# Performance work log

Measured on AMD Instinct MI355X. Metric: run time of the kernel, lower is better.

Reference implementation:

```python
import jax, jax.numpy as jnp
import numpy as np

B, N, C_IN = 8, 2048, 3
D = 64            # graph-conv feature dim
SPARSE_K = 8      # k_neighbors(16) * sparse_ratio(0.5)
LEVELS = 3        # wavelet_levels
H1, H2 = 256, 128 # fusion hidden dims

def _lin(key, fan_in, fan_out):
    k1, k2 = jax.random.split(key)
    s = 1.0 / np.sqrt(fan_in)
    W = jax.random.uniform(k1, (fan_in, fan_out), minval=-s, maxval=s, dtype=jnp.float32)
    b = jax.random.uniform(k2, (fan_out,), minval=-s, maxval=s, dtype=jnp.float32)
    return W, b

def setup_inputs() -> dict:
    key = jax.random.key(0)
    ks = jax.random.split(key, 12)
    x = jax.random.normal(ks[0], (B, N, C_IN), dtype=jnp.float32)
    W1, b1 = _lin(ks[1], C_IN, D)          # feature_transform
    W2, b2 = _lin(ks[2], 2 * D, D)         # edge_conv
    Ws1, bs1 = _lin(ks[3], C_IN, 64)       # suppressor layer 1
    Ws2, bs2 = _lin(ks[4], 64, LEVELS)     # suppressor layer 2
    Wf1, bf1 = _lin(ks[5], D * LEVELS, H1) # fusion
    Wf2, bf2 = _lin(ks[6], H1, H2)
    Wf3, bf3 = _lin(ks[7], H2, C_IN)
    ones = jnp.ones; zeros = jnp.zeros
    return {
        'x': x,
        'W1': W1, 'b1': b1, 'g1': ones((D,), jnp.float32), 'be1': zeros((D,), jnp.float32),
        'W2': W2, 'b2': b2, 'g2': ones((D,), jnp.float32), 'be2': zeros((D,), jnp.float32),
        'Ws1': Ws1, 'bs1': bs1, 'Ws2': Ws2, 'bs2': bs2,
        'Wf1': Wf1, 'bf1': bf1, 'gf1': ones((H1,), jnp.float32), 'bef1': zeros((H1,), jnp.float32),
        'Wf2': Wf2, 'bf2': bf2, 'gf2': ones((H2,), jnp.float32), 'bef2': zeros((H2,), jnp.float32),
        'Wf3': Wf3, 'bf3': bf3,
    }

def _leaky(v):
    return jnp.where(v > 0, v, 0.2 * v)

def reference(x, W1, b1, g1, be1, W2, b2, g2, be2, Ws1, bs1, Ws2, bs2,
              Wf1, bf1, gf1, bef1, Wf2, bf2, gf2, bef2, Wf3, bf3):
    # ---- AdaptiveSparseGraphConv ----
    # feature transform + eval-mode BN (running mean 0 / var 1 -> affine)
    feat = _leaky((x @ W1 + b1) * g1 + be1)                     # [B,N,D]
    # KNN via squared distances (monotonic in true cdist)
    x2 = jnp.sum(x * x, axis=-1)                                # [B,N]
    d2 = x2[:, :, None] + x2[:, None, :] - 2.0 * jnp.einsum('bnc,bmc->bnm', x, x)
    _, idx = jax.lax.top_k(-d2, SPARSE_K)                       # [B,N,k] nearest
    neighbor = jax.vmap(lambda f, i: f[i])(feat, idx)           # [B,N,k,D]
    edge = jnp.concatenate(
        [jnp.broadcast_to(feat[:, :, None, :], neighbor.shape), neighbor], axis=-1)  # [B,N,k,2D]
    conv = _leaky((edge @ W2 + b2) * g2 + be2)                  # [B,N,k,D]
    agg = jnp.max(conv, axis=2)                                 # [B,N,D]
    # ---- AdaptiveFrequencySupressor (per-point wavelet-level weights) ----
    fw = jax.nn.sigmoid(jax.nn.relu(x @ Ws1 + bs1) @ Ws2 + bs2) # [B,N,LEVELS]
    # frequency-adaptive multi-level weighting, concat across levels
    multi = (agg[:, :, None, :] * fw[:, :, :, None]).reshape(B, N, LEVELS * D)  # [B,N,LEVELS*D]
    # ---- EnhancedMultiScaleFusion (eval: dropout off, BN affine) ----
    h = _leaky((multi @ Wf1 + bf1) * gf1 + bef1)
    h = _leaky((h @ Wf2 + bf2) * gf2 + bef2)
    delta = h @ Wf3 + bf3                                       # [B,N,3]
    # ---- residual regularized output ----
    return x + 0.1 * delta
```

## Files before the change

kernel.cpp:

```cpp
#include <hip/hip_runtime.h>
#include <hip/hip_bf16.h>
#include <math.h>

#define BB   8
#define NN   2048
#define BN   16384
#define KNB  8

__device__ __forceinline__ float leaky(float v){ return v > 0.f ? v : 0.2f*v; }

using bf16x8 = __attribute__((ext_vector_type(8))) short;
using f32x16 = __attribute__((ext_vector_type(16))) float;

__global__ __launch_bounds__(256) void k_prep(
    const float* __restrict__ x,
    const float* __restrict__ Ws1, const float* __restrict__ bs1,
    const float* __restrict__ Ws2, const float* __restrict__ bs2,
    const float* __restrict__ Wf1, const float* __restrict__ Wf2,
    float* __restrict__ fw, __hip_bfloat16* __restrict__ Wf1T,
    __hip_bfloat16* __restrict__ Wf2T)
{
    int t = threadIdx.x;
    if (blockIdx.x < 4096) {
        int lane = t & 63;
        int p = blockIdx.x * 4 + (t >> 6);
        float x0 = x[p*3+0], x1 = x[p*3+1], x2 = x[p*3+2];
        int d = lane;
        float h = x0*Ws1[d] + x1*Ws1[64+d] + x2*Ws1[128+d] + bs1[d];
        h = fmaxf(h, 0.f);
        float s[3];
        #pragma unroll
        for (int l = 0; l < 3; ++l) {
            float v = h * Ws2[d*3 + l];
            #pragma unroll
            for (int off = 32; off; off >>= 1) v += __shfl_xor(v, off, 64);
            s[l] = v;
        }
        if (lane < 3) fw[p*3 + lane] = 1.f / (1.f + expf(-(s[lane] + bs2[lane])));
    } else if (blockIdx.x < 4120) {
        int base = (blockIdx.x - 4096) * 2048 + t * 8;
        #pragma unroll
        for (int j = 0; j < 8; ++j) {
            int e = base + j;
            int n = e / 192, k = e % 192;
            Wf1T[e] = __float2bfloat16(Wf1[k*256 + n]);
        }
    } else {
        int base = (blockIdx.x - 4120) * 2048 + t * 8;
        #pragma unroll
        for (int j = 0; j < 8; ++j) {
            int e = base + j;
            int n = e / 256, k = e % 256;
            Wf2T[e] = __float2bfloat16(Wf2[k*128 + n]);
        }
    }
}

#define CE64(a, b) { bool c_ = (b) < (a); unsigned long long mn_ = c_ ? (b) : (a); \
                     unsigned long long mx_ = c_ ? (a) : (b); (a) = mn_; (b) = mx_; }

__global__ __launch_bounds__(1024, 8) void k_knn(const float* __restrict__ x, int* __restrict__ idxo)
{
    __shared__ __align__(16) char smem[65536];
    float4*   sp  = (float4*)smem;
    unsigned* khi = (unsigned*)smem;
    unsigned* klo = (unsigned*)(smem + 32768);

    int t = threadIdx.x;
    int b = blockIdx.x >> 6;
    int qbase = (blockIdx.x & 63) * 32;
    int q = t & 31, seg = t >> 5;

    for (int i = t; i < NN; i += 1024) {
        float a = x[(b*NN + i)*3 + 0];
        float c = x[(b*NN + i)*3 + 1];
        float e = x[(b*NN + i)*3 + 2];
        sp[i] = make_float4(a, c, e, a*a + c*c + e*e);
    }
    __syncthreads();

    float4 qv = sp[qbase + q];

    unsigned long long R[8];
    #pragma unroll
    for (int j = 0; j < 8; ++j) R[j] = 0xFFFFFFFFFFFFFFFFull;

    int m0 = seg * 64;
    #pragma unroll 2
    for (int g = 0; g < 8; ++g) {
        unsigned long long S[8];
        #pragma unroll
        for (int jj = 0; jj < 8; ++jj) {
            int m = m0 + g*8 + jj;
            float4 v = sp[m];
            float s = qv.x*v.x; s = fmaf(qv.y, v.y, s); s = fmaf(qv.z, v.z, s);
            float d2 = fmaf(-2.f, s, qv.w + v.w);
            unsigned ub = __float_as_uint(d2);
            unsigned u  = ub ^ (unsigned)(((int)ub >> 31) | 0x80000000);
            S[jj] = ((unsigned long long)u << 32) | (unsigned)m;
        }
        CE64(S[0],S[1]); CE64(S[2],S[3]); CE64(S[4],S[5]); CE64(S[6],S[7]);
        CE64(S[0],S[2]); CE64(S[1],S[3]); CE64(S[4],S[6]); CE64(S[5],S[7]);
        CE64(S[1],S[2]); CE64(S[5],S[6]);
        CE64(S[0],S[4]); CE64(S[1],S[5]); CE64(S[2],S[6]); CE64(S[3],S[7]);
        CE64(S[2],S[4]); CE64(S[3],S[5]);
        CE64(S[1],S[2]); CE64(S[3],S[4]); CE64(S[5],S[6]);
        #pragma unroll
        for (int j = 0; j < 8; ++j) {
            unsigned long long bb = S[7-j];
            R[j] = R[j] < bb ? R[j] : bb;
        }
        CE64(R[0],R[4]); CE64(R[1],R[5]); CE64(R[2],R[6]); CE64(R[3],R[7]);
        CE64(R[0],R[2]); CE64(R[1],R[3]); CE64(R[4],R[6]); CE64(R[5],R[7]);
        CE64(R[0],R[1]); CE64(R[2],R[3]); CE64(R[4],R[5]); CE64(R[6],R[7]);
    }

    __syncthreads();
    #pragma unroll
    for (int j = 0; j < 8; ++j) {
        khi[j*1024 + t] = (unsigned)(R[j] >> 32);
        klo[j*1024 + t] = (unsigned)R[j];
    }

    for (int L = 32; L >= 2; L >>= 1) {
        __syncthreads();
        unsigned long long A[8], Bv[8];
        int p = t >> 5;
        bool active = (p < (L >> 1));
        if (active) {
            int rowA = (2*p)*32 + q, rowB = (2*p + 1)*32 + q;
            #pragma unroll
            for (int j = 0; j < 8; ++j) {
                A[j]  = ((unsigned long long)khi[j*1024 + rowA] << 32) | klo[j*1024 + rowA];
                Bv[j] = ((unsigned long long)khi[j*1024 + rowB] << 32) | klo[j*1024 + rowB];
            }
        }
        __syncthreads();
        if (active) {
            unsigned long long C[8];
            #pragma unroll
            for (int j = 0; j < 8; ++j) {
                unsigned long long bb = Bv[7-j];
                C[j] = A[j] < bb ? A[j] : bb;
            }
            CE64(C[0],C[4]); CE64(C[1],C[5]); CE64(C[2],C[6]); CE64(C[3],C[7]);
            CE64(C[0],C[2]); CE64(C[1],C[3]); CE64(C[4],C[6]); CE64(C[5],C[7]);
            CE64(C[0],C[1]); CE64(C[2],C[3]); CE64(C[4],C[5]); CE64(C[6],C[7]);
            if (L > 2) {
                int rowO = p*32 + q;
                #pragma unroll
                for (int j = 0; j < 8; ++j) {
                    khi[j*1024 + rowO] = (unsigned)(C[j] >> 32);
                    klo[j*1024 + rowO] = (unsigned)C[j];
                }
            } else {
                #pragma unroll
                for (int j = 0; j < 8; ++j)
                    idxo[(b*NN + qbase + q)*KNB + j] = b*NN + (int)(C[j] & 0xFFFFFFFFu);
            }
        }
    }
}

__global__ __launch_bounds__(256) void k_pq(
    const float* __restrict__ x,
    const float* __restrict__ W1, const float* __restrict__ b1,
    const float* __restrict__ g1, const float* __restrict__ be1,
    const float* __restrict__ W2, float* __restrict__ PQ)
{
    __shared__ float F_s[64*66];
    __shared__ float W_s[32*132];

    int t = threadIdx.x;
    int rb = blockIdx.x * 64;

    {
        int d = t & 63, g = t >> 6;
        float w0 = W1[d], w1 = W1[64+d], w2 = W1[128+d];
        float bb = b1[d], gg = g1[d], ee = be1[d];
        #pragma unroll 4
        for (int i = 0; i < 16; ++i) {
            int r = g*16 + i;
            const float* xp = &x[(rb + r)*3];
            float f = xp[0]*w0 + xp[1]*w1 + xp[2]*w2 + bb;
            f = leaky(f*gg + ee);
            F_s[r*66 + d] = f;
        }
    }

    int tx = t & 15, ty = t >> 4;
    float acc[4][8];
    #pragma unroll
    for (int i = 0; i < 4; ++i)
        #pragma unroll
        for (int j = 0; j < 8; ++j) acc[i][j] = 0.f;

    for (int k0 = 0; k0 < 64; k0 += 32) {
        __syncthreads();
        #pragma unroll
        for (int it = 0; it < 2; ++it) {
            int i2 = t + it*256;
            int k = i2 >> 4, c8 = (i2 & 15) * 8;
            const float* src = &W2[(k0 + k + (c8 >= 64 ? 64 : 0))*64 + (c8 & 63)];
            *(float4*)&W_s[k*132 + c8]     = *(const float4*)src;
            *(float4*)&W_s[k*132 + c8 + 4] = *(const float4*)(src + 4);
        }
        __syncthreads();
        #pragma unroll 4
        for (int kk = 0; kk < 32; ++kk) {
            float a[4];
            #pragma unroll
            for (int i = 0; i < 4; ++i) a[i] = F_s[(ty*4 + i)*66 + k0 + kk];
            float4 wA = *(const float4*)&W_s[kk*132 + tx*8];
            float4 wB = *(const float4*)&W_s[kk*132 + tx*8 + 4];
            #pragma unroll
            for (int i = 0; i < 4; ++i) {
                acc[i][0] = fmaf(a[i], wA.x, acc[i][0]);
                acc[i][1] = fmaf(a[i], wA.y, acc[i][1]);
                acc[i][2] = fmaf(a[i], wA.z, acc[i][2]);
                acc[i][3] = fmaf(a[i], wA.w, acc[i][3]);
                acc[i][4] = fmaf(a[i], wB.x, acc[i][4]);
                acc[i][5] = fmaf(a[i], wB.y, acc[i][5]);
                acc[i][6] = fmaf(a[i], wB.z, acc[i][6]);
                acc[i][7] = fmaf(a[i], wB.w, acc[i][7]);
            }
        }
    }

    #pragma unroll
    for (int i = 0; i < 4; ++i) {
        int r = rb + ty*4 + i;
        *(float4*)&PQ[r*128 + tx*8]     = make_float4(acc[i][0], acc[i][1], acc[i][2], acc[i][3]);
        *(float4*)&PQ[r*128 + tx*8 + 4] = make_float4(acc[i][4], acc[i][5], acc[i][6], acc[i][7]);
    }
}

__global__ __launch_bounds__(256) void k_agg(
    const float* __restrict__ PQ, const int* __restrict__ idx,
    const float* __restrict__ fw,
    const float* __restrict__ b2, const float* __restrict__ g2, const float* __restrict__ be2,
    __hip_bfloat16* __restrict__ multi)
{
    int lane = threadIdx.x & 63;
    int p = blockIdx.x * 4 + (threadIdx.x >> 6);
    float Pv = PQ[p*128 + lane] + b2[lane];
    float g = g2[lane], be = be2[lane];
    float mx = -1e30f;
    #pragma unroll
    for (int j = 0; j < KNB; ++j) {
        int nb = idx[p*KNB + j];
        float v = (Pv + PQ[nb*128 + 64 + lane]) * g + be;
        mx = fmaxf(mx, leaky(v));
    }
    float w0 = fw[p*3+0], w1 = fw[p*3+1], w2 = fw[p*3+2];
    multi[p*192 + lane]       = __float2bfloat16(mx * w0);
    multi[p*192 + 64  + lane] = __float2bfloat16(mx * w1);
    multi[p*192 + 128 + lane] = __float2bfloat16(mx * w2);
}

__global__ __launch_bounds__(256) void k_h1(
    const ushort* __restrict__ multi, const ushort* __restrict__ Wf1T,
    const float* __restrict__ bf1, const float* __restrict__ gf1,
    const float* __restrict__ bef1, __hip_bfloat16* __restrict__ h1)
{
    __shared__ ushort A_s[128*72];
    __shared__ ushort B_s[64*72];

    int t = threadIdx.x, w = t >> 6, lane = t & 63;
    int rb = blockIdx.x * 128, cb = blockIdx.y * 64;

    f32x16 acc[2];
    #pragma unroll
    for (int i = 0; i < 16; ++i) { acc[0][i] = 0.f; acc[1][i] = 0.f; }

    for (int k0 = 0; k0 < 192; k0 += 64) {
        #pragma unroll
        for (int it = 0; it < 4; ++it) {
            int i = t + it*256; int r = i >> 3, kq = (i & 7)*8;
            *(uint4*)&A_s[r*72 + kq] = *(const uint4*)&multi[(rb + r)*192 + k0 + kq];
        }
        #pragma unroll
        for (int it = 0; it < 2; ++it) {
            int i = t + it*256; int n = i >> 3, kq = (i & 7)*8;
            *(uint4*)&B_s[n*72 + kq] = *(const uint4*)&Wf1T[(cb + n)*192 + k0 + kq];
        }
        __syncthreads();
        int row = w*32 + (lane & 31);
        int kb = (lane >> 5)*8;
        #pragma unroll
        for (int s = 0; s < 4; ++s) {
            bf16x8 a  = *(const bf16x8*)&A_s[row*72 + s*16 + kb];
            bf16x8 b0 = *(const bf16x8*)&B_s[(lane & 31)*72 + s*16 + kb];
            bf16x8 b1 = *(const bf16x8*)&B_s[(32 + (lane & 31))*72 + s*16 + kb];
            acc[0] = __builtin_amdgcn_mfma_f32_32x32x16_bf16(a, b0, acc[0], 0, 0, 0);
            acc[1] = __builtin_amdgcn_mfma_f32_32x32x16_bf16(a, b1, acc[1], 0, 0, 0);
        }
        __syncthreads();
    }

    #pragma unroll
    for (int nb = 0; nb < 2; ++nb) {
        int c = cb + nb*32 + (lane & 31);
        float bv = bf1[c], gv = gf1[c], ev = bef1[c];
        #pragma unroll
        for (int r16 = 0; r16 < 16; ++r16) {
            int rr = (r16 & 3) + 8*(r16 >> 2) + 4*(lane >> 5);
            float v = leaky((acc[nb][r16] + bv)*gv + ev);
            h1[(rb + w*32 + rr)*256 + c] = __float2bfloat16(v);
        }
    }
}

__global__ __launch_bounds__(256) void k_h2out(
    const ushort* __restrict__ h1, const ushort* __restrict__ Wf2T,
    const float* __restrict__ bf2, const float* __restrict__ gf2,
    const float* __restrict__ bef2,
    const float* __restrict__ Wf3, const float* __restrict__ bf3,
    const float* __restrict__ x, float* __restrict__ out)
{
    __shared__ ushort A_s[128*72];
    __shared__ ushort B_s[128*72];

    int t = threadIdx.x, w = t >> 6, lane = t & 63;
    int rb = blockIdx.x * 128;

    f32x16 acc[4];
    #pragma unroll
    for (int nb = 0; nb < 4; ++nb)
        #pragma unroll
        for (int i = 0; i < 16; ++i) acc[nb][i] = 0.f;

    for (int k0 = 0; k0 < 256; k0 += 64) {
        #pragma unroll
        for (int it = 0; it < 4; ++it) {
            int i = t + it*256; int r = i >> 3, kq = (i & 7)*8;
            *(uint4*)&A_s[r*72 + kq] = *(const uint4*)&h1[(rb + r)*256 + k0 + kq];
        }
        #pragma unroll
        for (int it = 0; it < 4; ++it) {
            int i = t + it*256; int n = i >> 3, kq = (i & 7)*8;
            *(uint4*)&B_s[n*72 + kq] = *(const uint4*)&Wf2T[n*256 + k0 + kq];
        }
        __syncthreads();
        int row = w*32 + (lane & 31);
        int kb = (lane >> 5)*8;
        #pragma unroll
        for (int s = 0; s < 4; ++s) {
            bf16x8 a = *(const bf16x8*)&A_s[row*72 + s*16 + kb];
            #pragma unroll
            for (int nb = 0; nb < 4; ++nb) {
                bf16x8 b = *(const bf16x8*)&B_s[(nb*32 + (lane & 31))*72 + s*16 + kb];
                acc[nb] = __builtin_amdgcn_mfma_f32_32x32x16_bf16(a, b, acc[nb], 0, 0, 0);
            }
        }
        __syncthreads();
    }

    float bv[4], gv[4], ev[4], w3[4][3];
    #pragma unroll
    for (int nb = 0; nb < 4; ++nb) {
        int c = nb*32 + (lane & 31);
        bv[nb] = bf2[c]; gv[nb] = gf2[c]; ev[nb] = bef2[c];
        #pragma unroll
        for (int l = 0; l < 3; ++l) w3[nb][l] = Wf3[c*3 + l];
    }
    float b30 = bf3[0], b31 = bf3[1], b32 = bf3[2];

    #pragma unroll
    for (int r16 = 0; r16 < 16; ++r16) {
        float d0 = 0.f, d1 = 0.f, d2 = 0.f;
        #pragma unroll
        for (int nb = 0; nb < 4; ++nb) {
            float v = leaky((acc[nb][r16] + bv[nb])*gv[nb] + ev[nb]);
            d0 = fmaf(v, w3[nb][0], d0);
            d1 = fmaf(v, w3[nb][1], d1);
            d2 = fmaf(v, w3[nb][2], d2);
        }
        #pragma unroll
        for (int off = 16; off; off >>= 1) {
            d0 += __shfl_xor(d0, off, 64);
            d1 += __shfl_xor(d1, off, 64);
            d2 += __shfl_xor(d2, off, 64);
        }
        int row = rb + w*32 + (r16 & 3) + 8*(r16 >> 2) + 4*(lane >> 5);
        int l = lane & 31;
        if (l < 3) {
            float dl = (l == 0) ? d0 : (l == 1 ? d1 : d2);
            float bl = (l == 0) ? b30 : (l == 1 ? b31 : b32);
            out[row*3 + l] = x[row*3 + l] + 0.1f*(dl + bl);
        }
    }
}

extern "C" void kernel_launch(void* const* d_in, const int* in_sizes, int n_in,
                              void* d_out, int out_size, void* d_ws, size_t ws_size,
                              hipStream_t stream)
{
    const float* x    = (const float*)d_in[0];
    const float* W1   = (const float*)d_in[1];
    const float* b1   = (const float*)d_in[2];
    const float* g1   = (const float*)d_in[3];
    const float* be1  = (const float*)d_in[4];
    const float* W2   = (const float*)d_in[5];
    const float* b2   = (const float*)d_in[6];
    const float* g2   = (const float*)d_in[7];
    const float* be2  = (const float*)d_in[8];
    const float* Ws1  = (const float*)d_in[9];
    const float* bs1  = (const float*)d_in[10];
    const float* Ws2  = (const float*)d_in[11];
    const float* bs2  = (const float*)d_in[12];
    const float* Wf1  = (const float*)d_in[13];
    const float* bf1  = (const float*)d_in[14];
    const float* gf1  = (const float*)d_in[15];
    const float* bef1 = (const float*)d_in[16];
    const float* Wf2  = (const float*)d_in[17];
    const float* bf2  = (const float*)d_in[18];
    const float* gf2  = (const float*)d_in[19];
    const float* bef2 = (const float*)d_in[20];
    const float* Wf3  = (const float*)d_in[21];
    const float* bf3  = (const float*)d_in[22];
    float* out = (float*)d_out;

    char* ws = (char*)d_ws;
    float*          fw    = (float*)         (ws + 0);
    int*            idx   = (int*)           (ws + (1u  << 20));
    __hip_bfloat16* Wf1T  = (__hip_bfloat16*)(ws + (2u  << 20));
    __hip_bfloat16* Wf2T  = (__hip_bfloat16*)(ws + (3u  << 20));
    float*          PQ    = (float*)         (ws + (4u  << 20));
    __hip_bfloat16* multi = (__hip_bfloat16*)(ws + (12u << 20));
    __hip_bfloat16* h1    = (__hip_bfloat16*)(ws + (20u << 20));

    k_prep<<<4136, 256, 0, stream>>>(x, Ws1, bs1, Ws2, bs2, Wf1, Wf2, fw, Wf1T, Wf2T);
    k_knn<<<BB*64, 1024, 0, stream>>>(x, idx);
    k_pq<<<BN/64, 256, 0, stream>>>(x, W1, b1, g1, be1, W2, PQ);
    k_agg<<<BN/4, 256, 0, stream>>>(PQ, idx, fw, b2, g2, be2, multi);
    k_h1<<<dim3(BN/128, 4), 256, 0, stream>>>((const ushort*)multi, (const ushort*)Wf1T,
                                              bf1, gf1, bef1, h1);
    k_h2out<<<dim3(BN/128, 1), 256, 0, stream>>>((const ushort*)h1, (const ushort*)Wf2T,
                                                 bf2, gf2, bef2, Wf3, bf3, x, out);
}
```

Before: 180.5 us.

## Fuse prep into pq and agg kernels, store gathered Q half in bf16

Removes the standalone prep kernel: weight transposes move into extra blocks of the pq kernel, and the suppressor MLP that computes per-point level weights is computed inline in the aggregation kernel. The Q half of the edge-conv projection, which is gathered per neighbour, is stored in bf16 to halve gather traffic, while P stays fp32. The KNN key encoding is simplified by clamping distances to non-negative so the raw float bits sort correctly. This cuts one launch and the fw and PQ memory traffic, at the cost of bf16 rounding on neighbour features and recomputing the MLP per point in the aggregation kernel.

```diff
diff --git a/kernel.cpp b/kernel.cpp
--- a/kernel.cpp
+++ b/kernel.cpp
@@ -9,49 +9,118 @@
 
 __device__ __forceinline__ float leaky(float v){ return v > 0.f ? v : 0.2f*v; }
 
+__device__ __forceinline__ ushort f2bf(float f){
+    unsigned u = __float_as_uint(f);
+    return (ushort)((u + 0x7FFFu + ((u >> 16) & 1u)) >> 16);
+}
+__device__ __forceinline__ float bf2f(ushort h){
+    return __uint_as_float(((unsigned)h) << 16);
+}
+
 using bf16x8 = __attribute__((ext_vector_type(8))) short;
 using f32x16 = __attribute__((ext_vector_type(16))) float;
 
-__global__ __launch_bounds__(256) void k_prep(
+__global__ __launch_bounds__(256) void k_pq(
     const float* __restrict__ x,
-    const float* __restrict__ Ws1, const float* __restrict__ bs1,
-    const float* __restrict__ Ws2, const float* __restrict__ bs2,
+    const float* __restrict__ W1, const float* __restrict__ b1,
+    const float* __restrict__ g1, const float* __restrict__ be1,
+    const float* __restrict__ W2,
     const float* __restrict__ Wf1, const float* __restrict__ Wf2,
-    float* __restrict__ fw, __hip_bfloat16* __restrict__ Wf1T,
-    __hip_bfloat16* __restrict__ Wf2T)
+    float* __restrict__ P, ushort* __restrict__ Qb,
+    ushort* __restrict__ Wf1T, ushort* __restrict__ Wf2T)
 {
     int t = threadIdx.x;
-    if (blockIdx.x < 4096) {
-        int lane = t & 63;
-        int p = blockIdx.x * 4 + (t >> 6);
-        float x0 = x[p*3+0], x1 = x[p*3+1], x2 = x[p*3+2];
-        int d = lane;
-        float h = x0*Ws1[d] + x1*Ws1[64+d] + x2*Ws1[128+d] + bs1[d];
-        h = fmaxf(h, 0.f);
-        float s[3];
-        #pragma unroll
-        for (int l = 0; l < 3; ++l) {
-            float v = h * Ws2[d*3 + l];
-            #pragma unroll
-            for (int off = 32; off; off >>= 1) v += __shfl_xor(v, off, 64);
-            s[l] = v;
-        }
-        if (lane < 3) fw[p*3 + lane] = 1.f / (1.f + expf(-(s[lane] + bs2[lane])));
-    } else if (blockIdx.x < 4120) {
-        int base = (blockIdx.x - 4096) * 2048 + t * 8;
-        #pragma unroll
-        for (int j = 0; j < 8; ++j) {
-            int e = base + j;
-            int n = e / 192, k = e % 192;
-            Wf1T[e] = __float2bfloat16(Wf1[k*256 + n]);
-        }
-    } else {
-        int base = (blockIdx.x - 4120) * 2048 + t * 8;
-        #pragma unroll
-        for (int j = 0; j < 8; ++j) {
-            int e = base + j;
-            int n = e / 256, k = e % 256;
-            Wf2T[e] = __float2bfloat16(Wf2[k*128 + n]);
+    int bid = blockIdx.x;
+    if (bid >= 256) {
+        if (bid < 280) {
+            int base = (bid - 256) * 2048 + t * 8;
+            #pragma unroll
+            for (int j = 0; j < 8; ++j) {
+                int e = base + j;
+                int n = e / 192, k = e % 192;
+                Wf1T[e] = f2bf(Wf1[k*256 + n]);
+            }
+        } else {
+            int base = (bid - 280) * 2048 + t * 8;
+            #pragma unroll
+            for (int j = 0; j < 8; ++j) {
+                int e = base + j;
+                int n = e / 256, k = e % 256;
+                Wf2T[e] = f2bf(Wf2[k*128 + n]);
+            }
+        }
+        return;
+    }
+
+    __shared__ float F_s[64*66];
+    __shared__ float W_s[32*132];
+
+    int rb = bid * 64;
+
+    {
+        int d = t & 63, g = t >> 6;
+        float w0 = W1[d], w1 = W1[64+d], w2 = W1[128+d];
+        float bb = b1[d], gg = g1[d], ee = be1[d];
+        #pragma unroll 4
+        for (int i = 0; i < 16; ++i) {
+            int r = g*16 + i;
+            const float* xp = &x[(rb + r)*3];
+            float f = xp[0]*w0 + xp[1]*w1 + xp[2]*w2 + bb;
+            f = leaky(f*gg + ee);
+            F_s[r*66 + d] = f;
+        }
+    }
+
+    int tx = t & 15, ty = t >> 4;
+    float acc[4][8];
+    #pragma unroll
+    for (int i = 0; i < 4; ++i)
+        #pragma unroll
+        for (int j = 0; j < 8; ++j) acc[i][j] = 0.f;
+
+    for (int k0 = 0; k0 < 64; k0 += 32) {
+        __syncthreads();
+        #pragma unroll
+        for (int it = 0; it < 2; ++it) {
+            int i2 = t + it*256;
+            int k = i2 >> 4, c8 = (i2 & 15) * 8;
+            const float* src = &W2[(k0 + k + (c8 >= 64 ? 64 : 0))*64 + (c8 & 63)];
+            *(float4*)&W_s[k*132 + c8]     = *(const float4*)src;
+            *(float4*)&W_s[k*132 + c8 + 4] = *(const float4*)(src + 4);
+        }
+        __syncthreads();
+        #pragma unroll 4
+        for (int kk = 0; kk < 32; ++kk) {
+            float a[4];
+            #pragma unroll
+            for (int i = 0; i < 4; ++i) a[i] = F_s[(ty*4 + i)*66 + k0 + kk];
+            float4 wA = *(const float4*)&W_s[kk*132 + tx*8];
+            float4 wB = *(const float4*)&W_s[kk*132 + tx*8 + 4];
+            #pragma unroll
+            for (int i = 0; i < 4; ++i) {
+                acc[i][0] = fmaf(a[i], wA.x, acc[i][0]);
+                acc[i][1] = fmaf(a[i], wA.y, acc[i][1]);
+                acc[i][2] = fmaf(a[i], wA.z, acc[i][2]);
+                acc[i][3] = fmaf(a[i], wA.w, acc[i][3]);
+                acc[i][4] = fmaf(a[i], wB.x, acc[i][4]);
+                acc[i][5] = fmaf(a[i], wB.y, acc[i][5]);
+                acc[i][6] = fmaf(a[i], wB.z, acc[i][6]);
+                acc[i][7] = fmaf(a[i], wB.w, acc[i][7]);
+            }
+        }
+    }
+
+    #pragma unroll
+    for (int i = 0; i < 4; ++i) {
+        int r = rb + ty*4 + i;
+        if (tx < 8) {
+            *(float4*)&P[r*64 + tx*8]     = make_float4(acc[i][0], acc[i][1], acc[i][2], acc[i][3]);
+            *(float4*)&P[r*64 + tx*8 + 4] = make_float4(acc[i][4], acc[i][5], acc[i][6], acc[i][7]);
+        } else {
+            union { ushort u[8]; uint4 v; } pk;
+            #pragma unroll
+            for (int j = 0; j < 8; ++j) pk.u[j] = f2bf(acc[i][j]);
+            *(uint4*)&Qb[r*64 + (tx - 8)*8] = pk.v;
         }
     }
 }
@@ -95,8 +164,7 @@
             float4 v = sp[m];
             float s = qv.x*v.x; s = fmaf(qv.y, v.y, s); s = fmaf(qv.z, v.z, s);
             float d2 = fmaf(-2.f, s, qv.w + v.w);
-            unsigned ub = __float_as_uint(d2);
-            unsigned u  = ub ^ (unsigned)(((int)ub >> 31) | 0x80000000);
+            unsigned u = __float_as_uint(fmaxf(d2, 0.f));
             S[jj] = ((unsigned long long)u << 32) | (unsigned)m;
         }
         CE64(S[0],S[1]); CE64(S[2],S[3]); CE64(S[4],S[5]); CE64(S[6],S[7]);
@@ -162,106 +230,52 @@
     }
 }
 
-__global__ __launch_bounds__(256) void k_pq(
+__global__ __launch_bounds__(256) void k_agg(
     const float* __restrict__ x,
-    const float* __restrict__ W1, const float* __restrict__ b1,
-    const float* __restrict__ g1, const float* __restrict__ be1,
-    const float* __restrict__ W2, float* __restrict__ PQ)
-{
-    __shared__ float F_s[64*66];
-    __shared__ float W_s[32*132];
-
-    int t = threadIdx.x;
-    int rb = blockIdx.x * 64;
-
-    {
-        int d = t & 63, g = t >> 6;
-        float w0 = W1[d], w1 = W1[64+d], w2 = W1[128+d];
-        float bb = b1[d], gg = g1[d], ee = be1[d];
-        #pragma unroll 4
-        for (int i = 0; i < 16; ++i) {
-            int r = g*16 + i;
-            const float* xp = &x[(rb + r)*3];
-            float f = xp[0]*w0 + xp[1]*w1 + xp[2]*w2 + bb;
-            f = leaky(f*gg + ee);
-            F_s[r*66 + d] = f;
-        }
-    }
-
-    int tx = t & 15, ty = t >> 4;
-    float acc[4][8];
-    #pragma unroll
-    for (int i = 0; i < 4; ++i)
-        #pragma unroll
-        for (int j = 0; j < 8; ++j) acc[i][j] = 0.f;
-
-    for (int k0 = 0; k0 < 64; k0 += 32) {
-        __syncthreads();
-        #pragma unroll
-        for (int it = 0; it < 2; ++it) {
-            int i2 = t + it*256;
-            int k = i2 >> 4, c8 = (i2 & 15) * 8;
-            const float* src = &W2[(k0 + k + (c8 >= 64 ? 64 : 0))*64 + (c8 & 63)];
-            *(float4*)&W_s[k*132 + c8]     = *(const float4*)src;
-            *(float4*)&W_s[k*132 + c8 + 4] = *(const float4*)(src + 4);
-        }
-        __syncthreads();
-        #pragma unroll 4
-        for (int kk = 0; kk < 32; ++kk) {
-            float a[4];
-            #pragma unroll
-            for (int i = 0; i < 4; ++i) a[i] = F_s[(ty*4 + i)*66 + k0 + kk];
-            float4 wA = *(const float4*)&W_s[kk*132 + tx*8];
-            float4 wB = *(const float4*)&W_s[kk*132 + tx*8 + 4];
-            #pragma unroll
-            for (int i = 0; i < 4; ++i) {
-                acc[i][0] = fmaf(a[i], wA.x, acc[i][0]);
-                acc[i][1] = fmaf(a[i], wA.y, acc[i][1]);
-                acc[i][2] = fmaf(a[i], wA.z, acc[i][2]);
-                acc[i][3] = fmaf(a[i], wA.w, acc[i][3]);
-                acc[i][4] = fmaf(a[i], wB.x, acc[i][4]);
-                acc[i][5] = fmaf(a[i], wB.y, acc[i][5]);
-                acc[i][6] = fmaf(a[i], wB.z, acc[i][6]);
-                acc[i][7] = fmaf(a[i], wB.w, acc[i][7]);
-            }
-        }
-    }
-
-    #pragma unroll
-    for (int i = 0; i < 4; ++i) {
-        int r = rb + ty*4 + i;
-        *(float4*)&PQ[r*128 + tx*8]     = make_float4(acc[i][0], acc[i][1], acc[i][2], acc[i][3]);
-        *(float4*)&PQ[r*128 + tx*8 + 4] = make_float4(acc[i][4], acc[i][5], acc[i][6], acc[i][7]);
-    }
-}
-
-__global__ __launch_bounds__(256) void k_agg(
-    const float* __restrict__ PQ, const int* __restrict__ idx,
-    const float* __restrict__ fw,
-    const float* __restrict__ b2, const float* __restrict__ g2, const float* __restrict__ be2,
-    __hip_bfloat16* __restrict__ multi)
+    const float* __restrict__ P, const ushort* __restrict__ Qb,
+    const int* __restrict__ idx,
+    const float* __restrict__ Ws1, const float* __restrict__ bs1,
+    const float* __restrict__ Ws2, const float* __restrict__ bs2,
+    const float* __restrict__ b2, const float* __restrict__ g2,
+    const float* __restrict__ be2,
+    ushort* __restrict__ multi)
 {
     int lane = threadIdx.x & 63;
     int p = blockIdx.x * 4 + (threadIdx.x >> 6);
-    float Pv = PQ[p*128 + lane] + b2[lane];
+
+    float x0 = x[p*3+0], x1 = x[p*3+1], x2 = x[p*3+2];
+    float h = fmaxf(x0*Ws1[lane] + x1*Ws1[64+lane] + x2*Ws1[128+lane] + bs1[lane], 0.f);
+    float s[3];
+    #pragma unroll
+    for (int l = 0; l < 3; ++l) {
+        float v = h * Ws2[lane*3 + l];
+        #pragma unroll
+        for (int off = 32; off; off >>= 1) v += __shfl_xor(v, off, 64);
+        s[l] = v + bs2[l];
+    }
+    float fw0 = 1.f/(1.f + expf(-s[0]));
+    float fw1 = 1.f/(1.f + expf(-s[1]));
+    float fw2 = 1.f/(1.f + expf(-s[2]));
+
+    float Pv = P[p*64 + lane] + b2[lane];
     float g = g2[lane], be = be2[lane];
     float mx = -1e30f;
     #pragma unroll
     for (int j = 0; j < KNB; ++j) {
         int nb = idx[p*KNB + j];
-        float v = (Pv + PQ[nb*128 + 64 + lane]) * g + be;
+        float qv = bf2f(Qb[nb*64 + lane]);
+        float v = (Pv + qv) * g + be;
         mx = fmaxf(mx, leaky(v));
     }
-    float w0 = fw[p*3+0], w1 = fw[p*3+1], w2 = fw[p*3+2];
-    multi[p*192 + lane]       = __float2bfloat16(mx * w0);
-    multi[p*192 + 64  + lane] = __float2bfloat16(mx * w1);
-    multi[p*192 + 128 + lane] = __float2bfloat16(mx * w2);
+    multi[p*192 + lane]       = f2bf(mx * fw0);
+    multi[p*192 + 64  + lane] = f2bf(mx * fw1);
+    multi[p*192 + 128 + lane] = f2bf(mx * fw2);
 }
 
 __global__ __launch_bounds__(256) void k_h1(
     const ushort* __restrict__ multi, const ushort* __restrict__ Wf1T,
     const float* __restrict__ bf1, const float* __restrict__ gf1,
-    const float* __restrict__ bef1, __hip_bfloat16* __restrict__ h1)
+    const float* __restrict__ bef1, ushort* __restrict__ h1)
 {
     __shared__ ushort A_s[128*72];
     __shared__ ushort B_s[64*72];
@@ -306,7 +320,7 @@
         for (int r16 = 0; r16 < 16; ++r16) {
             int rr = (r16 & 3) + 8*(r16 >> 2) + 4*(lane >> 5);
             float v = leaky((acc[nb][r16] + bv)*gv + ev);
-            h1[(rb + w*32 + rr)*256 + c] = __float2bfloat16(v);
+            h1[(rb + w*32 + rr)*256 + c] = f2bf(v);
         }
     }
 }
@@ -422,20 +436,17 @@
     float* out = (float*)d_out;
 
     char* ws = (char*)d_ws;
-    float*          fw    = (float*)         (ws + 0);
-    int*            idx   = (int*)           (ws + (1u  << 20));
-    __hip_bfloat16* Wf1T  = (__hip_bfloat16*)(ws + (2u  << 20));
-    __hip_bfloat16* Wf2T  = (__hip_bfloat16*)(ws + (3u  << 20));
-    float*          PQ    = (float*)         (ws + (4u  << 20));
-    __hip_bfloat16* multi = (__hip_bfloat16*)(ws + (12u << 20));
-    __hip_bfloat16* h1    = (__hip_bfloat16*)(ws + (20u << 20));
-
-    k_prep<<<4136, 256, 0, stream>>>(x, Ws1, bs1, Ws2, bs2, Wf1, Wf2, fw, Wf1T, Wf2T);
+    int*    idx   = (int*)   (ws + 0);
+    ushort* Wf1T  = (ushort*)(ws + (1u << 20));
+    ushort* Wf2T  = (ushort*)(ws + (1u << 20) + (512u << 10));
+    float*  P     = (float*) (ws + (2u  << 20));
+    ushort* Qb    = (ushort*)(ws + (6u  << 20));
+    ushort* multi = (ushort*)(ws + (8u  << 20));
+    ushort* h1    = (ushort*)(ws + (14u << 20));
+
+    k_pq<<<296, 256, 0, stream>>>(x, W1, b1, g1, be1, W2, Wf1, Wf2, P, Qb, Wf1T, Wf2T);
     k_knn<<<BB*64, 1024, 0, stream>>>(x, idx);
-    k_pq<<<BN/64, 256, 0, stream>>>(x, W1, b1, g1, be1, W2, PQ);
-    k_agg<<<BN/4, 256, 0, stream>>>(PQ, idx, fw, b2, g2, be2, multi);
-    k_h1<<<dim3(BN/128, 4), 256, 0, stream>>>((const ushort*)multi, (const ushort*)Wf1T,
-                                              bf1, gf1, bef1, h1);
-    k_h2out<<<dim3(BN/128, 1), 256, 0, stream>>>((const ushort*)h1, (const ushort*)Wf2T,
-                                                 bf2, gf2, bef2, Wf3, bf3, x, out);
-}
+    k_agg<<<BN/4, 256, 0, stream>>>(x, P, Qb, idx, Ws1, bs1, Ws2, bs2, b2, g2, be2, multi);
+    k_h1<<<dim3(BN/128, 4), 256, 0, stream>>>(multi, Wf1T, bf1, gf1, bef1, h1);
+    k_h2out<<<dim3(BN/128, 1), 256, 0, stream>>>(h1, Wf2T, bf2, gf2, bef2, Wf3, bf3, x, out);
+}
```

New measurement: 176.7 us. 1.02x faster.
